# Kernel tuning notes

Measured on AMD Instinct MI355X. Metric: run time of the kernel, lower is better.

The kernel has to match this reference:

```python
import jax, jax.numpy as jnp
import numpy as np

NUM_HEADS = 16
WINDOW = 256


def setup_inputs() -> dict:
    key = jax.random.key(0)
    ks = jax.random.split(key, 4)
    B, S, D = 1, 4096, 1024
    scale = 1.0 / np.sqrt(D)  # keep logits sane with random weights
    x = jax.random.normal(ks[0], (B, S, D), dtype=jnp.float32)
    Wq = jax.random.normal(ks[1], (D, D), dtype=jnp.float32) * scale
    Wk = jax.random.normal(ks[2], (D, D), dtype=jnp.float32) * scale
    Wv = jax.random.normal(ks[3], (D, D), dtype=jnp.float32) * scale
    bq = jnp.zeros((D,), dtype=jnp.float32)
    bk = jnp.zeros((D,), dtype=jnp.float32)
    bv = jnp.zeros((D,), dtype=jnp.float32)
    return {"x": x, "Wq": Wq, "bq": bq, "Wk": Wk, "bk": bk, "Wv": Wv, "bv": bv}


def reference(x, Wq, bq, Wk, bk, Wv, bv):
    B, S, D = x.shape
    H = NUM_HEADS
    depth = D // H

    def split_heads(t):
        return t.reshape(B, S, H, depth).transpose(0, 2, 1, 3)  # [B,H,S,depth]

    # torch nn.Linear: y = x @ W.T + b
    Q = split_heads(x @ Wq.T + bq)
    K = split_heads(x @ Wk.T + bk)
    V = split_heads(x @ Wv.T + bv)

    scores = jnp.einsum("bhqd,bhkd->bhqk", Q, K) / jnp.sqrt(jnp.float32(depth))
    idx = jnp.arange(S)
    band = jnp.abs(idx[None, :] - idx[:, None]) <= WINDOW  # [S,S] local window
    scores = jnp.where(band[None, None], scores, -jnp.inf)
    attn = jax.nn.softmax(scores, axis=-1)
    out = jnp.einsum("bhqk,bhkd->bhqd", attn, V)
    return out.transpose(0, 2, 1, 3).reshape(B, S, D)
```

## Files before the change

kernel.cpp:

```cpp
#include <hip/hip_runtime.h>
#include <hip/hip_bf16.h>

typedef __attribute__((ext_vector_type(4))) float f32x4;
typedef __attribute__((ext_vector_type(16))) float f32x16;
typedef __attribute__((ext_vector_type(8))) short s16x8;
typedef __attribute__((ext_vector_type(4))) float float4_t;
typedef __attribute__((ext_vector_type(2))) unsigned int u32x2;

union U8 { s16x8 v; unsigned u[4]; };

__device__ __forceinline__ ushort f2bf(float f) {
  union { float f; unsigned u; } v; v.f = f;
  unsigned r = v.u + 0x7fffu + ((v.u >> 16) & 1u);
  return (ushort)(r >> 16);
}

__device__ __forceinline__ void async_copy16(ushort* lds, const ushort* g) {
  __builtin_amdgcn_global_load_lds(
      (const __attribute__((address_space(1))) unsigned int*)g,
      (__attribute__((address_space(3))) unsigned int*)lds, 16, 0, 0);
}

__device__ __forceinline__ unsigned lds_addr(const void* p) {
  return (unsigned)(unsigned long long)(__attribute__((address_space(3))) const void*)p;
}

#define TRRD(dst, addr, off_lit) \
  asm volatile("ds_read_b64_tr_b16 %0, %1 offset:" #off_lit : "=v"(dst) : "v"(addr))

__global__ __launch_bounds__(256) void convert_kernel(
    const float* __restrict__ x, const float* __restrict__ Wq,
    const float* __restrict__ Wk, const float* __restrict__ Wv,
    ushort* __restrict__ xs, ushort* __restrict__ ws) {
  int b = blockIdx.x;
  if (b < 2048) {
    int c = b * 256 + threadIdx.x;
    int kc = c & 127;
    int m = c >> 7;
    const float4_t* s = (const float4_t*)&x[(size_t)m * 1024 + kc * 8];
    float4_t a0 = s[0], a1 = s[1];
    s16x8 v;
    v[0] = (short)f2bf(a0[0]); v[1] = (short)f2bf(a0[1]);
    v[2] = (short)f2bf(a0[2]); v[3] = (short)f2bf(a0[3]);
    v[4] = (short)f2bf(a1[0]); v[5] = (short)f2bf(a1[1]);
    v[6] = (short)f2bf(a1[2]); v[7] = (short)f2bf(a1[3]);
    int tm = m >> 7, tk = kc >> 3, r = m & 127, c8 = kc & 7;
    *(s16x8*)&xs[((size_t)(tm * 16 + tk) * 128 + r) * 64 + ((c8 ^ (r & 7)) * 8)] = v;
  } else {
    int c = (b - 2048) * 256 + threadIdx.x;
    int kc = c & 127;
    int n = c >> 7;
    int p = n >> 10, nW = n & 1023;
    const float* __restrict__ W = (p == 0) ? Wq : (p == 1) ? Wk : Wv;
    const float4_t* s = (const float4_t*)&W[(size_t)nW * 1024 + kc * 8];
    float4_t a0 = s[0], a1 = s[1];
    s16x8 v;
    v[0] = (short)f2bf(a0[0]); v[1] = (short)f2bf(a0[1]);
    v[2] = (short)f2bf(a0[2]); v[3] = (short)f2bf(a0[3]);
    v[4] = (short)f2bf(a1[0]); v[5] = (short)f2bf(a1[1]);
    v[6] = (short)f2bf(a1[2]); v[7] = (short)f2bf(a1[3]);
    unsigned tn3 = (unsigned)n / 192u;
    unsigned r = (unsigned)n - tn3 * 192u;
    int tk = kc >> 3, c8 = kc & 7;
    *(s16x8*)&ws[((size_t)(tn3 * 16 + tk) * 192 + r) * 64 + ((c8 ^ (r & 7)) * 8)] = v;
  }
}

__global__ __launch_bounds__(512, 2) void qkv_gemm_kernel(
    const ushort* __restrict__ xs, const ushort* __restrict__ wsb,
    const float* __restrict__ bq, const float* __restrict__ bk,
    const float* __restrict__ bv, ushort* __restrict__ qkv) {
  __shared__ ushort lA[2][16384];
  __shared__ ushort lB[2][12288];
  const int t = threadIdx.x;
  const int lane = t & 63, w = t >> 6;
  const int wm = w >> 1, wn = w & 1;
  const int l15 = lane & 15, l4 = lane >> 4;
  const int phys = blockIdx.x;
  const int swz = (phys & 7) * 32 + (phys >> 3);
  const int xcd = swz >> 5, jj = swz & 31;
  const int bm = (xcd >> 1) * 4 + (jj >> 3);
  const int bn = (xcd & 1) * 8 + (jj & 7);

  const ushort* Apan = xs + (size_t)(2 * bm) * 16 * 8192;
  const ushort* Bpan = wsb + (size_t)bn * 16 * 12288;

  f32x4 acc[4][6];
#pragma unroll
  for (int i = 0; i < 4; i++)
#pragma unroll
    for (int j = 0; j < 6; j++) acc[i][j] = (f32x4)0.f;

#define STAGE_A(buf, kt)                                                        \
  do {                                                                          \
    const ushort* s0 = Apan + (size_t)(kt) * 8192;                              \
    const ushort* s1 = Apan + (size_t)(16 + (kt)) * 8192;                       \
    async_copy16(&lA[buf][t * 8], s0 + t * 8);                                  \
    async_copy16(&lA[buf][(t + 512) * 8], s0 + (t + 512) * 8);                  \
    async_copy16(&lA[buf][8192 + t * 8], s1 + t * 8);                           \
    async_copy16(&lA[buf][8192 + (t + 512) * 8], s1 + (t + 512) * 8);           \
  } while (0)
#define STAGE_B(buf, kt)                                                        \
  do {                                                                          \
    const ushort* s2 = Bpan + (size_t)(kt) * 12288;                             \
    async_copy16(&lB[buf][t * 8], s2 + t * 8);                                  \
    async_copy16(&lB[buf][(t + 512) * 8], s2 + (t + 512) * 8);                  \
    async_copy16(&lB[buf][(t + 1024) * 8], s2 + (t + 1024) * 8);                \
  } while (0)

  STAGE_A(0, 0);
  STAGE_B(0, 0);
  asm volatile("s_waitcnt vmcnt(0)");
  __builtin_amdgcn_s_barrier();

  for (int kt = 0; kt < 16; ++kt) {
    const int cur = kt & 1;
    s16x8 a0[4], a1[4], b0[6], b1[6];
#pragma unroll
    for (int mi = 0; mi < 4; mi++) {
      int ra = wm * 64 + mi * 16 + l15;
      a0[mi] = *(const s16x8*)&lA[cur][ra * 64 + (l4 ^ (ra & 7)) * 8];
      a1[mi] = *(const s16x8*)&lA[cur][ra * 64 + ((4 + l4) ^ (ra & 7)) * 8];
    }
#pragma unroll
    for (int ni = 0; ni < 6; ni++) {
      int rb = wn * 96 + ni * 16 + l15;
      b0[ni] = *(const s16x8*)&lB[cur][rb * 64 + (l4 ^ (rb & 7)) * 8];
      b1[ni] = *(const s16x8*)&lB[cur][rb * 64 + ((4 + l4) ^ (rb & 7)) * 8];
    }
    if (kt + 1 < 16) {
      STAGE_A(cur ^ 1, kt + 1);
      STAGE_B(cur ^ 1, kt + 1);
    }
#pragma unroll
    for (int mi = 0; mi < 4; mi++)
#pragma unroll
      for (int ni = 0; ni < 6; ni++) {
        acc[mi][ni] = __builtin_amdgcn_mfma_f32_16x16x32_bf16(a0[mi], b0[ni], acc[mi][ni], 0, 0, 0);
        acc[mi][ni] = __builtin_amdgcn_mfma_f32_16x16x32_bf16(a1[mi], b1[ni], acc[mi][ni], 0, 0, 0);
      }
    asm volatile("s_waitcnt vmcnt(0) lgkmcnt(0)" ::: "memory");
    __builtin_amdgcn_s_barrier();
  }
#undef STAGE_A
#undef STAGE_B

#pragma unroll
  for (int ni = 0; ni < 6; ni++) {
    int col = bn * 192 + wn * 96 + ni * 16 + l15;
    int p = col >> 10;
    const float* bias = (p == 0) ? bq : (p == 1) ? bk : bv;
    float b = bias[col & 1023];
    float qscale = (p == 0) ? 0.125f * 1.44269504f : 1.0f;
    int h = (col >> 6) & 15, dd = col & 63;
    size_t base = ((size_t)(p * 16 + h) * 4096) * 64 + dd;
#pragma unroll
    for (int mi = 0; mi < 4; mi++) {
#pragma unroll
      for (int r = 0; r < 4; r++) {
        int s = bm * 256 + wm * 64 + mi * 16 + l4 * 4 + r;
        float v = (acc[mi][ni][r] + b) * qscale;
        qkv[base + (size_t)s * 64] = f2bf(v);
      }
    }
  }
}

__global__ __launch_bounds__(256) void attn_local_kernel(
    const ushort* __restrict__ qkv, float* __restrict__ out) {
  __shared__ ushort lds[2][2][4096];
  const int bid = blockIdx.x;
  const int wid = (bid & 7) * 64 + (bid >> 3);
  const int hd = wid >> 5;
  const int q0 = (wid & 31) << 7;
  const int t = threadIdx.x;
  const int lane = t & 63, w = t >> 6;
  const int l15 = lane & 15, l31 = lane & 31;
  const int b4 = (lane >> 4) & 1, hf = lane >> 5;
  const int qw = q0 + w * 32;
  const int myq = qw + l31;

  const ushort* __restrict__ Q = qkv;
  const ushort* __restrict__ K = qkv + (size_t)16 * 4096 * 64;
  const ushort* __restrict__ V = K + (size_t)16 * 4096 * 64;

  s16x8 qf[4];
  {
    const ushort* qp = &Q[((size_t)hd * 4096 + myq) * 64];
#pragma unroll
    for (int kc = 0; kc < 4; kc++) qf[kc] = *(const s16x8*)&qp[16 * kc + 8 * hf];
  }

  U8 ones;
  {
    unsigned w1 = (l31 == 0) ? 0x3F803F80u : 0u;
    ones.u[0] = w1; ones.u[1] = w1; ones.u[2] = w1; ones.u[3] = w1;
  }

  f32x16 oa0 = (f32x16)0.f, oa1 = (f32x16)0.f, oden = (f32x16)0.f;
  float mrow = -1e30f;

  const unsigned vtr0 = lds_addr(&lds[0][1][0]) +
      (unsigned)(hf * 1024 + (l15 >> 2) * 128 + b4 * 32 + (l15 & 3) * 8);

  int kstart = q0 - 256; if (kstart < 0) kstart = 0;
  int kend = q0 + 384; if (kend > 4096) kend = 4096;

#define STAGE_KV(buf, kb)                                                      \
  do {                                                                         \
    const ushort* Kg = &K[((size_t)hd * 4096 + (kb)) * 64];                    \
    const ushort* Vg = &V[((size_t)hd * 4096 + (kb)) * 64];                    \
    _Pragma("unroll") for (int i = 0; i < 2; i++) {                            \
      int off = i * 2048 + t * 8;                                              \
      int row = off >> 6;                                                      \
      int c8s = (off >> 3) & 7;                                                \
      async_copy16(&lds[buf][0][off], &Kg[row * 64 + ((c8s ^ (row & 7)) * 8)]);\
      async_copy16(&lds[buf][1][off], &Vg[off]);                               \
    }                                                                          \
  } while (0)

  STAGE_KV(0, kstart);
  asm volatile("s_waitcnt vmcnt(0)");
  __builtin_amdgcn_s_barrier();

  for (int kb = kstart; kb < kend; kb += 64) {
    const int cur = ((kb - kstart) >> 6) & 1;
    if (kb + 64 < kend) {
      if (cur) STAGE_KV(0, kb + 64); else STAGE_KV(1, kb + 64);
    }
    bool active = (kb + 63 >= qw - 256) && (kb <= qw + 31 + 256);
    if (active) {
      const ushort* lK = &lds[cur][0][0];
      f32x16 st0 = (f32x16)0.f, st1 = (f32x16)0.f;
      __builtin_amdgcn_s_setprio(1);
#pragma unroll
      for (int kc = 0; kc < 4; kc++) {
        int c8 = 2 * kc + hf;
        int r0 = l31;
        s16x8 kf0 = *(const s16x8*)&lK[r0 * 64 + ((c8 ^ (r0 & 7)) * 8)];
        st0 = __builtin_amdgcn_mfma_f32_32x32x16_bf16(kf0, qf[kc], st0, 0, 0, 0);
        int r1 = 32 + l31;
        s16x8 kf1 = *(const s16x8*)&lK[r1 * 64 + ((c8 ^ (r1 & 7)) * 8)];
        st1 = __builtin_amdgcn_mfma_f32_32x32x16_bf16(kf1, qf[kc], st1, 0, 0, 0);
      }
      __builtin_amdgcn_s_setprio(0);
      const bool interior = (kb >= qw - 225) && (kb <= qw + 193);
      if (!interior) {
        int base0 = myq - kb - 4 * hf + 256;
#pragma unroll
        for (int r = 0; r < 16; r++) {
          int ko = (r & 3) + 8 * (r >> 2);
          if (!((unsigned)(base0 - ko) <= 512u)) st0[r] = -3e38f;
          if (!((unsigned)(base0 - 32 - ko) <= 512u)) st1[r] = -3e38f;
        }
      }
      float rm;
      {
        float a = fmaxf(fmaxf(st0[0], st0[1]), fmaxf(st0[2], st0[3]));
        float b = fmaxf(fmaxf(st0[4], st0[5]), fmaxf(st0[6], st0[7]));
        float c = fmaxf(fmaxf(st0[8], st0[9]), fmaxf(st0[10], st0[11]));
        float d = fmaxf(fmaxf(st0[12], st0[13]), fmaxf(st0[14], st0[15]));
        float e = fmaxf(fmaxf(st1[0], st1[1]), fmaxf(st1[2], st1[3]));
        float f = fmaxf(fmaxf(st1[4], st1[5]), fmaxf(st1[6], st1[7]));
        float g = fmaxf(fmaxf(st1[8], st1[9]), fmaxf(st1[10], st1[11]));
        float h2 = fmaxf(fmaxf(st1[12], st1[13]), fmaxf(st1[14], st1[15]));
        rm = fmaxf(fmaxf(fmaxf(a, b), fmaxf(c, d)), fmaxf(fmaxf(e, f), fmaxf(g, h2)));
      }
      rm = fmaxf(rm, __shfl_xor(rm, 32));
      if (__any(rm > mrow + 8.0f)) {
        float mn = fmaxf(mrow, rm);
        float sc = __builtin_amdgcn_exp2f(mrow - mn);
        mrow = mn;
        int srcB = (lane & 32); srcB += srcB >> 3;
#pragma unroll
        for (int r = 0; r < 16; r++) {
          float scr = __shfl(sc, srcB + (r & 3) + 8 * (r >> 2));
          oa0[r] *= scr; oa1[r] *= scr; oden[r] *= scr;
        }
      }
      const unsigned vtr = vtr0 + (unsigned)cur * 16384u;
      u32x2 v0, v1, v2, v3, v4, v5, v6, v7, v8, v9, v10, v11, v12, v13, v14, v15;
      TRRD(v0, vtr, 0);     TRRD(v1, vtr, 512);  TRRD(v2, vtr, 64);    TRRD(v3, vtr, 576);
      TRRD(v4, vtr, 2048);  TRRD(v5, vtr, 2560); TRRD(v6, vtr, 2112);  TRRD(v7, vtr, 2624);
      TRRD(v8, vtr, 4096);  TRRD(v9, vtr, 4608); TRRD(v10, vtr, 4160); TRRD(v11, vtr, 4672);
      TRRD(v12, vtr, 6144); TRRD(v13, vtr, 6656); TRRD(v14, vtr, 6208); TRRD(v15, vtr, 6720);
      U8 pa0, pa1, pa2, pa3;
#define PACK(STV, RB, OUT)                                                     \
  do {                                                                         \
    float e0 = __builtin_amdgcn_exp2f(STV[RB + 0] - mrow);                     \
    float e1 = __builtin_amdgcn_exp2f(STV[RB + 1] - mrow);                     \
    float e2 = __builtin_amdgcn_exp2f(STV[RB + 2] - mrow);                     \
    float e3 = __builtin_amdgcn_exp2f(STV[RB + 3] - mrow);                     \
    float e4 = __builtin_amdgcn_exp2f(STV[RB + 4] - mrow);                     \
    float e5 = __builtin_amdgcn_exp2f(STV[RB + 5] - mrow);                     \
    float e6 = __builtin_amdgcn_exp2f(STV[RB + 6] - mrow);                     \
    float e7 = __builtin_amdgcn_exp2f(STV[RB + 7] - mrow);                     \
    unsigned a0, a1, b0, b1;                                                   \
    asm("v_cvt_pk_bf16_f32 %0, %1, %2" : "=v"(a0) : "v"(e0), "v"(e1));         \
    asm("v_cvt_pk_bf16_f32 %0, %1, %2" : "=v"(a1) : "v"(e2), "v"(e3));         \
    asm("v_cvt_pk_bf16_f32 %0, %1, %2" : "=v"(b0) : "v"(e4), "v"(e5));         \
    asm("v_cvt_pk_bf16_f32 %0, %1, %2" : "=v"(b1) : "v"(e6), "v"(e7));         \
    asm volatile("v_permlane32_swap_b32 %0, %1" : "+v"(a0), "+v"(b0));         \
    asm volatile("v_permlane32_swap_b32 %0, %1" : "+v"(a1), "+v"(b1));         \
    OUT.u[0] = a0; OUT.u[1] = a1; OUT.u[2] = b0; OUT.u[3] = b1;                \
  } while (0)
      PACK(st0, 0, pa0); PACK(st0, 8, pa1); PACK(st1, 0, pa2); PACK(st1, 8, pa3);
#undef PACK
#define MFMA3(PA, VA0, VA1, VB0, VB1)                                          \
  do {                                                                         \
    U8 f0, f1;                                                                 \
    f0.u[0] = VA0[0]; f0.u[1] = VA0[1]; f0.u[2] = VA1[0]; f0.u[3] = VA1[1];    \
    f1.u[0] = VB0[0]; f1.u[1] = VB0[1]; f1.u[2] = VB1[0]; f1.u[3] = VB1[1];    \
    __builtin_amdgcn_s_setprio(1);                                             \
    oa0 = __builtin_amdgcn_mfma_f32_32x32x16_bf16(PA.v, f0.v, oa0, 0, 0, 0);   \
    oa1 = __builtin_amdgcn_mfma_f32_32x32x16_bf16(PA.v, f1.v, oa1, 0, 0, 0);   \
    oden = __builtin_amdgcn_mfma_f32_32x32x16_bf16(PA.v, ones.v, oden, 0, 0, 0);\
    __builtin_amdgcn_s_setprio(0);                                             \
  } while (0)
      asm volatile("s_waitcnt lgkmcnt(12)");
      __builtin_amdgcn_sched_barrier(0);
      MFMA3(pa0, v0, v1, v2, v3);
      asm volatile("s_waitcnt lgkmcnt(8)");
      __builtin_amdgcn_sched_barrier(0);
      MFMA3(pa1, v4, v5, v6, v7);
      asm volatile("s_waitcnt lgkmcnt(4)");
      __builtin_amdgcn_sched_barrier(0);
      MFMA3(pa2, v8, v9, v10, v11);
      asm volatile("s_waitcnt lgkmcnt(0)");
      __builtin_amdgcn_sched_barrier(0);
      MFMA3(pa3, v12, v13, v14, v15);
#undef MFMA3
    }
    asm volatile("s_waitcnt vmcnt(0)");
    __builtin_amdgcn_s_barrier();
  }
#undef STAGE_KV
#pragma unroll
  for (int r = 0; r < 16; r++) {
    float den = __shfl(oden[r], lane & 32);
    float linv = 1.0f / den;
    int s = qw + (r & 3) + 8 * (r >> 2) + 4 * hf;
    out[(size_t)s * 1024 + hd * 64 + l31] = oa0[r] * linv;
    out[(size_t)s * 1024 + hd * 64 + 32 + l31] = oa1[r] * linv;
  }
}

extern "C" void kernel_launch(void* const* d_in, const int* in_sizes, int n_in,
                              void* d_out, int out_size, void* d_ws, size_t ws_size,
                              hipStream_t stream) {
  const float* x  = (const float*)d_in[0];
  const float* Wq = (const float*)d_in[1];
  const float* bq = (const float*)d_in[2];
  const float* Wk = (const float*)d_in[3];
  const float* bk = (const float*)d_in[4];
  const float* Wv = (const float*)d_in[5];
  const float* bv = (const float*)d_in[6];

  ushort* qkv = (ushort*)d_ws;
  ushort* xs  = (ushort*)((char*)d_ws + (size_t)25165824);
  ushort* wsb = xs + (size_t)4096 * 1024;
  float* out = (float*)d_out;

  convert_kernel<<<3584, 256, 0, stream>>>(x, Wq, Wk, Wv, xs, wsb);
  qkv_gemm_kernel<<<256, 512, 0, stream>>>(xs, wsb, bq, bk, bv, qkv);
  attn_local_kernel<<<512, 256, 0, stream>>>(qkv, out);
}
```

Measured before the change: 66.68 us.

## Retile QKV GEMM to 256x256 blocks with 8-phase split-K pipelined staging

Changes the QKV projection GEMM from 256x192 tiles on 256 blocks to 256x256 tiles on 192 blocks, with each block's 8 waves arranged 2x4. The bf16 pre-conversion layout is rewritten into 256-row panels split into two 32-wide K halves with a new XOR swizzle. The main loop becomes an 8-phase schedule that interleaves small async LDS loads with MFMA batches, uses partial vmcnt waits and setprio, and prefetches up to two K-steps ahead. The goal is more reuse per tile and overlap of global loads with compute. The cost is fewer blocks than CUs (192) and more barriers per K-step.

```diff
diff --git a/kernel.cpp b/kernel.cpp
--- a/kernel.cpp
+++ b/kernel.cpp
@@ -31,7 +31,7 @@
 __global__ __launch_bounds__(256) void convert_kernel(
     const float* __restrict__ x, const float* __restrict__ Wq,
     const float* __restrict__ Wk, const float* __restrict__ Wv,
-    ushort* __restrict__ xs, ushort* __restrict__ ws) {
+    ushort* __restrict__ xs, ushort* __restrict__ wsb) {
   int b = blockIdx.x;
   if (b < 2048) {
     int c = b * 256 + threadIdx.x;
@@ -44,25 +44,27 @@
     v[2] = (short)f2bf(a0[2]); v[3] = (short)f2bf(a0[3]);
     v[4] = (short)f2bf(a1[0]); v[5] = (short)f2bf(a1[1]);
     v[6] = (short)f2bf(a1[2]); v[7] = (short)f2bf(a1[3]);
-    int tm = m >> 7, tk = kc >> 3, r = m & 127, c8 = kc & 7;
-    *(s16x8*)&xs[((size_t)(tm * 16 + tk) * 128 + r) * 64 + ((c8 ^ (r & 7)) * 8)] = v;
+    int tm = m >> 8, row = m & 255;
+    int kt = kc >> 3, kh = (kc >> 2) & 1, cg = kc & 3;
+    int cs = cg ^ ((row >> 1) & 3);
+    *(s16x8*)&xs[((((size_t)(tm * 16 + kt) * 2 + kh) * 256 + row) * 4 + cs) * 8] = v;
   } else {
     int c = (b - 2048) * 256 + threadIdx.x;
     int kc = c & 127;
     int n = c >> 7;
-    int p = n >> 10, nW = n & 1023;
+    int p = n >> 10;
     const float* __restrict__ W = (p == 0) ? Wq : (p == 1) ? Wk : Wv;
-    const float4_t* s = (const float4_t*)&W[(size_t)nW * 1024 + kc * 8];
+    const float4_t* s = (const float4_t*)&W[(size_t)(n & 1023) * 1024 + kc * 8];
     float4_t a0 = s[0], a1 = s[1];
     s16x8 v;
     v[0] = (short)f2bf(a0[0]); v[1] = (short)f2bf(a0[1]);
     v[2] = (short)f2bf(a0[2]); v[3] = (short)f2bf(a0[3]);
     v[4] = (short)f2bf(a1[0]); v[5] = (short)f2bf(a1[1]);
     v[6] = (short)f2bf(a1[2]); v[7] = (short)f2bf(a1[3]);
-    unsigned tn3 = (unsigned)n / 192u;
-    unsigned r = (unsigned)n - tn3 * 192u;
-    int tk = kc >> 3, c8 = kc & 7;
-    *(s16x8*)&ws[((size_t)(tn3 * 16 + tk) * 192 + r) * 64 + ((c8 ^ (r & 7)) * 8)] = v;
+    int tn = n >> 8, row = n & 255;
+    int kt = kc >> 3, kh = (kc >> 2) & 1, cg = kc & 3;
+    int cs = cg ^ ((row >> 1) & 3);
+    *(s16x8*)&wsb[((((size_t)(tn * 16 + kt) * 2 + kh) * 256 + row) * 4 + cs) * 8] = v;
   }
 }
 
@@ -70,84 +72,90 @@
     const ushort* __restrict__ xs, const ushort* __restrict__ wsb,
     const float* __restrict__ bq, const float* __restrict__ bk,
     const float* __restrict__ bv, ushort* __restrict__ qkv) {
-  __shared__ ushort lA[2][16384];
-  __shared__ ushort lB[2][12288];
+  __shared__ ushort lA[2][2][8192];
+  __shared__ ushort lB[2][2][8192];
   const int t = threadIdx.x;
   const int lane = t & 63, w = t >> 6;
-  const int wm = w >> 1, wn = w & 1;
+  const int wm = w >> 2, wn = w & 3;
   const int l15 = lane & 15, l4 = lane >> 4;
   const int phys = blockIdx.x;
-  const int swz = (phys & 7) * 32 + (phys >> 3);
-  const int xcd = swz >> 5, jj = swz & 31;
-  const int bm = (xcd >> 1) * 4 + (jj >> 3);
-  const int bn = (xcd & 1) * 8 + (jj & 7);
-
-  const ushort* Apan = xs + (size_t)(2 * bm) * 16 * 8192;
-  const ushort* Bpan = wsb + (size_t)bn * 16 * 12288;
-
-  f32x4 acc[4][6];
-#pragma unroll
-  for (int i = 0; i < 4; i++)
-#pragma unroll
-    for (int j = 0; j < 6; j++) acc[i][j] = (f32x4)0.f;
-
-#define STAGE_A(buf, kt)                                                        \
-  do {                                                                          \
-    const ushort* s0 = Apan + (size_t)(kt) * 8192;                              \
-    const ushort* s1 = Apan + (size_t)(16 + (kt)) * 8192;                       \
-    async_copy16(&lA[buf][t * 8], s0 + t * 8);                                  \
-    async_copy16(&lA[buf][(t + 512) * 8], s0 + (t + 512) * 8);                  \
-    async_copy16(&lA[buf][8192 + t * 8], s1 + t * 8);                           \
-    async_copy16(&lA[buf][8192 + (t + 512) * 8], s1 + (t + 512) * 8);           \
-  } while (0)
-#define STAGE_B(buf, kt)                                                        \
-  do {                                                                          \
-    const ushort* s2 = Bpan + (size_t)(kt) * 12288;                             \
-    async_copy16(&lB[buf][t * 8], s2 + t * 8);                                  \
-    async_copy16(&lB[buf][(t + 512) * 8], s2 + (t + 512) * 8);                  \
-    async_copy16(&lB[buf][(t + 1024) * 8], s2 + (t + 1024) * 8);                \
-  } while (0)
-
-  STAGE_A(0, 0);
-  STAGE_B(0, 0);
-  asm volatile("s_waitcnt vmcnt(0)");
+  const int swz = (phys & 7) * 24 + (phys >> 3);
+  const int bm = swz / 12, bn = swz - (swz / 12) * 12;
+
+  const ushort* Apan = xs + (size_t)bm * 16 * 2 * 8192;
+  const ushort* Bpan = wsb + (size_t)bn * 16 * 2 * 8192;
+
+  f32x4 acc[8][4];
+#pragma unroll
+  for (int i = 0; i < 8; i++)
+#pragma unroll
+    for (int j = 0; j < 4; j++) acc[i][j] = (f32x4)0.f;
+
+#define STG_A(d, kh, kt)                                                       \
+  do {                                                                         \
+    const ushort* s_ = Apan + ((size_t)(kt) * 2 + (kh)) * 8192;                \
+    async_copy16(&lA[d][kh][t * 8], s_ + t * 8);                               \
+    async_copy16(&lA[d][kh][(t + 512) * 8], s_ + (t + 512) * 8);               \
+  } while (0)
+#define STG_B(d, kh, kt)                                                       \
+  do {                                                                         \
+    const ushort* s_ = Bpan + ((size_t)(kt) * 2 + (kh)) * 8192;                \
+    async_copy16(&lB[d][kh][t * 8], s_ + t * 8);                               \
+    async_copy16(&lB[d][kh][(t + 512) * 8], s_ + (t + 512) * 8);               \
+  } while (0)
+
+  STG_A(0, 0, 0); STG_B(0, 0, 0);
+  STG_A(0, 1, 0); STG_B(0, 1, 0);
+  STG_A(1, 0, 1); STG_B(1, 0, 1);
+  asm volatile("s_waitcnt vmcnt(8)" ::: "memory");
   __builtin_amdgcn_s_barrier();
 
-  for (int kt = 0; kt < 16; ++kt) {
-    const int cur = kt & 1;
-    s16x8 a0[4], a1[4], b0[6], b1[6];
-#pragma unroll
-    for (int mi = 0; mi < 4; mi++) {
-      int ra = wm * 64 + mi * 16 + l15;
-      a0[mi] = *(const s16x8*)&lA[cur][ra * 64 + (l4 ^ (ra & 7)) * 8];
-      a1[mi] = *(const s16x8*)&lA[cur][ra * 64 + ((4 + l4) ^ (ra & 7)) * 8];
-    }
-#pragma unroll
-    for (int ni = 0; ni < 6; ni++) {
-      int rb = wn * 96 + ni * 16 + l15;
-      b0[ni] = *(const s16x8*)&lB[cur][rb * 64 + (l4 ^ (rb & 7)) * 8];
-      b1[ni] = *(const s16x8*)&lB[cur][rb * 64 + ((4 + l4) ^ (rb & 7)) * 8];
-    }
-    if (kt + 1 < 16) {
-      STAGE_A(cur ^ 1, kt + 1);
-      STAGE_B(cur ^ 1, kt + 1);
-    }
-#pragma unroll
-    for (int mi = 0; mi < 4; mi++)
-#pragma unroll
-      for (int ni = 0; ni < 6; ni++) {
-        acc[mi][ni] = __builtin_amdgcn_mfma_f32_16x16x32_bf16(a0[mi], b0[ni], acc[mi][ni], 0, 0, 0);
-        acc[mi][ni] = __builtin_amdgcn_mfma_f32_16x16x32_bf16(a1[mi], b1[ni], acc[mi][ni], 0, 0, 0);
-      }
-    asm volatile("s_waitcnt vmcnt(0) lgkmcnt(0)" ::: "memory");
-    __builtin_amdgcn_s_barrier();
-  }
-#undef STAGE_A
-#undef STAGE_B
-
-#pragma unroll
-  for (int ni = 0; ni < 6; ni++) {
-    int col = bn * 192 + wn * 96 + ni * 16 + l15;
+#define PHASE(P, STAGE_STMT)                                                   \
+  do {                                                                         \
+    const int d_ = (P) >> 2, kk_ = ((P) >> 1) & 1, qr_ = (P) & 1;              \
+    s16x8 af[4], bf[4];                                                        \
+    _Pragma("unroll") for (int i_ = 0; i_ < 4; i_++) {                         \
+      int r_ = wm * 128 + qr_ * 64 + i_ * 16 + l15;                            \
+      af[i_] = *(const s16x8*)&lA[d_][kk_][r_ * 32 + ((l4 ^ ((r_ >> 1) & 3)) * 8)]; \
+      int c_ = wn * 64 + i_ * 16 + l15;                                        \
+      bf[i_] = *(const s16x8*)&lB[d_][kk_][c_ * 32 + ((l4 ^ ((c_ >> 1) & 3)) * 8)]; \
+    }                                                                          \
+    STAGE_STMT;                                                                \
+    __builtin_amdgcn_s_barrier();                                              \
+    asm volatile("s_waitcnt lgkmcnt(0)" ::: "memory");                         \
+    __builtin_amdgcn_sched_barrier(0);                                         \
+    __builtin_amdgcn_s_setprio(1);                                             \
+    _Pragma("unroll") for (int ri_ = 0; ri_ < 4; ri_++)                        \
+      _Pragma("unroll") for (int ci_ = 0; ci_ < 4; ci_++)                      \
+        acc[qr_ * 4 + ri_][ci_] = __builtin_amdgcn_mfma_f32_16x16x32_bf16(     \
+            af[ri_], bf[ci_], acc[qr_ * 4 + ri_][ci_], 0, 0, 0);               \
+    __builtin_amdgcn_s_setprio(0);                                             \
+    if ((P) & 1) {                                                             \
+      if (last) asm volatile("s_waitcnt vmcnt(0)" ::: "memory");               \
+      else      asm volatile("s_waitcnt vmcnt(8)" ::: "memory");               \
+    }                                                                          \
+    __builtin_amdgcn_s_barrier();                                              \
+  } while (0)
+
+  for (int i = 0; i < 8; ++i) {
+    const bool last = (i == 7);
+    const int kt1 = 2 * i + 1, kt2 = 2 * i + 2, kt3 = 2 * i + 3;
+    PHASE(0, STG_A(1, 1, kt1));
+    PHASE(1, STG_B(1, 1, kt1));
+    PHASE(2, if (!last) STG_A(0, 0, kt2));
+    PHASE(3, if (!last) STG_B(0, 0, kt2));
+    PHASE(4, if (!last) STG_A(0, 1, kt2));
+    PHASE(5, if (!last) STG_B(0, 1, kt2));
+    PHASE(6, if (!last) STG_A(1, 0, kt3));
+    PHASE(7, if (!last) STG_B(1, 0, kt3));
+  }
+#undef PHASE
+#undef STG_A
+#undef STG_B
+
+#pragma unroll
+  for (int ci = 0; ci < 4; ci++) {
+    int col = bn * 256 + wn * 64 + ci * 16 + l15;
     int p = col >> 10;
     const float* bias = (p == 0) ? bq : (p == 1) ? bk : bv;
     float b = bias[col & 1023];
@@ -155,11 +163,11 @@
     int h = (col >> 6) & 15, dd = col & 63;
     size_t base = ((size_t)(p * 16 + h) * 4096) * 64 + dd;
 #pragma unroll
-    for (int mi = 0; mi < 4; mi++) {
+    for (int ri = 0; ri < 8; ri++) {
 #pragma unroll
       for (int r = 0; r < 4; r++) {
-        int s = bm * 256 + wm * 64 + mi * 16 + l4 * 4 + r;
-        float v = (acc[mi][ni][r] + b) * qscale;
+        int s = bm * 256 + wm * 128 + (ri >> 2) * 64 + (ri & 3) * 16 + l4 * 4 + r;
+        float v = (acc[ri][ci][r] + b) * qscale;
         qkv[base + (size_t)s * 64] = f2bf(v);
       }
     }
@@ -358,10 +366,10 @@
 
   ushort* qkv = (ushort*)d_ws;
   ushort* xs  = (ushort*)((char*)d_ws + (size_t)25165824);
-  ushort* wsb = xs + (size_t)4096 * 1024;
+  ushort* wsb = xs + (size_t)16 * 16 * 2 * 8192;
   float* out = (float*)d_out;
 
   convert_kernel<<<3584, 256, 0, stream>>>(x, Wq, Wk, Wv, xs, wsb);
-  qkv_gemm_kernel<<<256, 512, 0, stream>>>(xs, wsb, bq, bk, bv, qkv);
+  qkv_gemm_kernel<<<192, 512, 0, stream>>>(xs, wsb, bq, bk, bv, qkv);
   attn_local_kernel<<<512, 256, 0, stream>>>(qkv, out);
 }
```

After: 74.62 us. 1.12x slower.
